# Kernel tuning notes

Measured on AMD Instinct MI355X. Metric: run time of the kernel, lower is better.

Reference implementation:

```python
import jax, jax.numpy as jnp
import numpy as np

N = 10000        # nodes
E = 160000       # edges (avg degree 16)
WIDTH = 32       # node hidden width
KER_W = 256      # kernel MLP hidden width
KER_IN = 6       # edge feature dim
DEPTH = 4        # message-passing iterations


def setup_inputs() -> dict:
    key = jax.random.key(0)
    ks = jax.random.split(key, 12)
    def w(k, shape, fan_in):
        return jax.random.normal(k, shape, jnp.float32) * (1.0 / np.sqrt(fan_in)).astype(np.float32)
    return {
        "x": jax.random.normal(ks[0], (N, 1), jnp.float32),
        "edge_index": jax.random.randint(ks[1], (2, E), 0, N),
        "edge_attr": jax.random.uniform(ks[2], (E, KER_IN), dtype=jnp.float32),
        # fc1: Linear(1, WIDTH)
        "fc1_w": w(ks[3], (1, WIDTH), 1), "fc1_b": jnp.zeros((WIDTH,), jnp.float32),
        # kernel DenseNet: KER_IN -> KER_W -> KER_W -> WIDTH^2 (ReLU between, none after last)
        "k1_w": w(ks[4], (KER_IN, KER_W), KER_IN), "k1_b": jnp.zeros((KER_W,), jnp.float32),
        "k2_w": w(ks[5], (KER_W, KER_W), KER_W), "k2_b": jnp.zeros((KER_W,), jnp.float32),
        "k3_w": w(ks[6], (KER_W, WIDTH * WIDTH), KER_W), "k3_b": jnp.zeros((WIDTH * WIDTH,), jnp.float32),
        # NNConv root weight + bias
        "root_w": w(ks[7], (WIDTH, WIDTH), WIDTH), "conv_b": jnp.zeros((WIDTH,), jnp.float32),
        # fc2: Linear(WIDTH, 1)
        "fc2_w": w(ks[8], (WIDTH, 1), WIDTH), "fc2_b": jnp.zeros((1,), jnp.float32),
    }


def reference(x, edge_index, edge_attr, fc1_w, fc1_b, k1_w, k1_b, k2_w, k2_b,
              k3_w, k3_b, root_w, conv_b, fc2_w, fc2_b):
    src, dst = edge_index[0], edge_index[1]  # messages flow src -> dst

    # Per-edge kernel weights (edge_attr is constant across depth -> compute once).
    h = jax.nn.relu(edge_attr @ k1_w + k1_b)
    h = jax.nn.relu(h @ k2_w + k2_b)
    W_e = (h @ k3_w + k3_b).reshape(E, WIDTH, WIDTH)  # [E, in, out]

    # Degree for scatter-mean (avoid div by zero).
    deg = jax.ops.segment_sum(jnp.ones((E,), jnp.float32), dst, num_segments=N)
    inv_deg = (1.0 / jnp.maximum(deg, 1.0))[:, None]

    h_node = x @ fc1_w + fc1_b  # [N, WIDTH]
    for _ in range(DEPTH):
        msg = jnp.einsum('ei,eio->eo', h_node[src], W_e)              # gather + per-edge GEMM
        agg = jax.ops.segment_sum(msg, dst, num_segments=N) * inv_deg  # scatter-mean
        h_node = jax.nn.relu(agg + h_node @ root_w + conv_b)
    return h_node @ fc2_w + fc2_b  # [N, 1]
```

## Files before the change

kernel.cpp:

```cpp
#include <hip/hip_runtime.h>
#include <hip/hip_fp16.h>

#define NNODE 10000
#define NEDGE 160000
#define W32 32
#define BSTR 40
#define PANEL_F16 10240
#define PANEL3_F16 5120
#define UB_TILES 20000
#define HB_STR 264
#define TB_STR 1036

typedef _Float16 f16;
typedef _Float16 f16x4 __attribute__((ext_vector_type(4)));
typedef _Float16 f16x8 __attribute__((ext_vector_type(8)));
typedef float f32x4 __attribute__((ext_vector_type(4)));

__device__ __forceinline__ void stage_panel(f16* lds, const f16* g, int w, int lane) {
    #pragma unroll
    for (int i = 0; i < 5; ++i) {
        int slot = w * 320 + i * 64 + lane;
        __builtin_amdgcn_global_load_lds(
            (const __attribute__((address_space(1))) unsigned int*)(g + (size_t)slot * 8),
            (__attribute__((address_space(3))) unsigned int*)(lds + (size_t)(w * 320 + i * 64) * 8),
            16, 0, 0);
    }
}

__device__ __forceinline__ void stage_panel10k(f16* lds, const f16* g, int w, int lane) {
    #pragma unroll
    for (int i = 0; i < 2; ++i) {
        int base = i * 256 + w * 64;
        __builtin_amdgcn_global_load_lds(
            (const __attribute__((address_space(1))) unsigned int*)(g + (size_t)(base + lane) * 8),
            (__attribute__((address_space(3))) unsigned int*)(lds + (size_t)base * 8),
            16, 0, 0);
    }
    if (w < 2) {
        int base = 512 + w * 64;
        __builtin_amdgcn_global_load_lds(
            (const __attribute__((address_space(1))) unsigned int*)(g + (size_t)(base + lane) * 8),
            (__attribute__((address_space(3))) unsigned int*)(lds + (size_t)base * 8),
            16, 0, 0);
    }
}

__global__ __launch_bounds__(256) void pack_k1(const float* __restrict__ k1w, f16* __restrict__ k1p) {
    int t = blockIdx.x * 256 + threadIdx.x;
    int j = t / BSTR, c = t % BSTR;
    k1p[t] = (c < 6) ? (f16)k1w[c * 256 + j] : (f16)0.f;
}
__global__ __launch_bounds__(256) void pack_k2(const float* __restrict__ k2w, f16* __restrict__ k2p) {
    int t = blockIdx.x * 256 + threadIdx.x;
    int kk = t / PANEL_F16, r = t % PANEL_F16;
    int j = r / BSTR, c = r % BSTR;
    k2p[t] = (c < 32) ? (f16)k2w[(size_t)(kk * 32 + c) * 256 + j] : (f16)0.f;
}
__global__ __launch_bounds__(256) void pack_k3(const float* __restrict__ k3w, f16* __restrict__ k3p) {
    int t = blockIdx.x * 256 + threadIdx.x;
    int p = t / PANEL3_F16, r = t % PANEL3_F16;
    int np = p >> 3, kk = p & 7;
    int j = r / BSTR, c = r % BSTR;
    k3p[t] = (c < 32) ? (f16)k3w[(size_t)(kk * 32 + c) * 1024 + np * 128 + j] : (f16)0.f;
}
__global__ __launch_bounds__(256) void pack_k3t(const float* __restrict__ k3w, f16* __restrict__ k3t) {
    int t = blockIdx.x * 256 + threadIdx.x;
    int q = t / BSTR, i = t % BSTR;
    int o = q >> 8, c = q & 255;
    k3t[t] = (i < 32) ? (f16)k3w[(size_t)c * 1024 + i * 32 + o] : (f16)0.f;
}

__global__ __launch_bounds__(256) void h2_kernel(
    const float* __restrict__ ea,
    const f16* __restrict__ k1p, const float* __restrict__ k1b,
    const f16* __restrict__ k2p, const float* __restrict__ k2b,
    f16* __restrict__ h2c, int e_start, const int* __restrict__ remap)
{
    __shared__ __align__(16) f16 bls[2][256 * BSTR];
    __shared__ __align__(16) f16 ea_s[64 * BSTR];
    __shared__ __align__(16) f16 hbuf[64 * HB_STR];

    const int t = threadIdx.x, w = t >> 6, lane = t & 63, quad = lane >> 4, l15 = lane & 15;
    const int el0 = blockIdx.x * 64;
    const int e0 = e_start + el0;

    stage_panel(bls[0], k1p, w, lane);
    for (int i = t; i < 64 * BSTR; i += 256) {
        int e = i / BSTR, c = i % BSTR;
        ea_s[i] = (f16)((c < 6) ? ea[(size_t)(e0 + e) * 6 + c] : 0.f);
    }
    __syncthreads();

    f16x8 a1 = *(const f16x8*)&ea_s[(w * 16 + l15) * BSTR + quad * 8];
    {
        f32x4 acc1[16];
        #pragma unroll
        for (int nt = 0; nt < 16; ++nt) { float b = k1b[nt * 16 + l15]; acc1[nt] = (f32x4){b, b, b, b}; }
        stage_panel(bls[1], k2p, w, lane);
        #pragma unroll
        for (int nt = 0; nt < 16; ++nt) {
            f16x8 bf = *(const f16x8*)&bls[0][(nt * 16 + l15) * BSTR + quad * 8];
            acc1[nt] = __builtin_amdgcn_mfma_f32_16x16x32_f16(a1, bf, acc1[nt], 0, 0, 0);
        }
        #pragma unroll
        for (int nt = 0; nt < 16; ++nt)
            #pragma unroll
            for (int r = 0; r < 4; ++r)
                hbuf[(w * 16 + quad * 4 + r) * HB_STR + nt * 16 + l15] = (f16)fmaxf(acc1[nt][r], 0.f);
    }
    __syncthreads();

    const int mh = w & 1, nh = w >> 1;
    f16x8 a2[2][8];
    #pragma unroll
    for (int m = 0; m < 2; ++m)
        #pragma unroll
        for (int kk = 0; kk < 8; ++kk)
            a2[m][kk] = *(const f16x8*)&hbuf[(mh * 32 + m * 16 + l15) * HB_STR + kk * 32 + quad * 8];
    f32x4 acc[2][8];
    #pragma unroll
    for (int nt = 0; nt < 8; ++nt) {
        float b = k2b[nh * 128 + nt * 16 + l15];
        acc[0][nt] = (f32x4){b, b, b, b};
        acc[1][nt] = (f32x4){b, b, b, b};
    }
    for (int kk = 0; kk < 8; ++kk) {
        if (kk < 7)
            stage_panel(bls[kk & 1], k2p + (size_t)(kk + 1) * PANEL_F16, w, lane);
        const f16* B = bls[(kk + 1) & 1];
        #pragma unroll
        for (int nt = 0; nt < 8; ++nt) {
            f16x8 bf = *(const f16x8*)&B[(nh * 128 + nt * 16 + l15) * BSTR + quad * 8];
            acc[0][nt] = __builtin_amdgcn_mfma_f32_16x16x32_f16(a2[0][kk], bf, acc[0][nt], 0, 0, 0);
            acc[1][nt] = __builtin_amdgcn_mfma_f32_16x16x32_f16(a2[1][kk], bf, acc[1][nt], 0, 0, 0);
        }
        __syncthreads();
    }
    size_t orow[2][4];
    #pragma unroll
    for (int m = 0; m < 2; ++m)
        #pragma unroll
        for (int r = 0; r < 4; ++r) {
            int row = mh * 32 + m * 16 + quad * 4 + r;
            orow[m][r] = remap ? (size_t)remap[e0 + row] : (size_t)(el0 + row);
        }
    #pragma unroll
    for (int m = 0; m < 2; ++m)
        #pragma unroll
        for (int nt = 0; nt < 8; ++nt)
            #pragma unroll
            for (int r = 0; r < 4; ++r)
                h2c[orow[m][r] * 256 + nh * 128 + nt * 16 + l15] = (f16)fmaxf(acc[m][nt][r], 0.f);
}

__global__ __launch_bounds__(256) void hist_kernel(const int* __restrict__ ei, int* __restrict__ cnt) {
    int e = blockIdx.x * 256 + threadIdx.x;
    if (e < NEDGE) atomicAdd(&cnt[ei[e]], 1);
}
__global__ __launch_bounds__(256) void scan_kernel(
    const int* __restrict__ cnt, int* __restrict__ edgeStart,
    int* __restrict__ tileStartN, int* __restrict__ cursor)
{
    __shared__ int pE[256], pT[256];
    const int t = threadIdx.x;
    int se = 0, st = 0;
    for (int k = 0; k < 40; ++k) {
        int n = t * 40 + k;
        if (n < NNODE) { int c = cnt[n]; se += c; st += (c + 15) >> 4; }
    }
    pE[t] = se; pT[t] = st;
    __syncthreads();
    if (t == 0) {
        int aE = 0, aT = 0;
        for (int i = 0; i < 256; ++i) { int tE = pE[i], tT = pT[i]; pE[i] = aE; pT[i] = aT; aE += tE; aT += tT; }
        tileStartN[NNODE] = aT;
    }
    __syncthreads();
    int oE = pE[t], oT = pT[t];
    for (int k = 0; k < 40; ++k) {
        int n = t * 40 + k;
        if (n < NNODE) {
            edgeStart[n] = oE; cursor[n] = oE; tileStartN[n] = oT;
            int c = cnt[n]; oE += c; oT += (c + 15) >> 4;
        }
    }
}
__global__ __launch_bounds__(256) void scatter_kernel(
    const int* __restrict__ ei, int* __restrict__ cursor,
    int* __restrict__ dstS, int* __restrict__ sortpos)
{
    int e = blockIdx.x * 256 + threadIdx.x;
    if (e < NEDGE) {
        int s = ei[e];
        int p = atomicAdd(&cursor[s], 1);
        dstS[p] = ei[NEDGE + e];
        sortpos[e] = p;
    }
}
__global__ __launch_bounds__(256) void tiles_kernel(
    const int* __restrict__ cnt, const int* __restrict__ edgeStart, const int* __restrict__ tileStartN,
    int* __restrict__ tileNode, int* __restrict__ tileE0, int* __restrict__ tileCnt)
{
    int n = blockIdx.x * 256 + threadIdx.x;
    if (n < NNODE) {
        int d = cnt[n], t0 = tileStartN[n], e0 = edgeStart[n];
        for (int k = 0; k * 16 < d; ++k) {
            int rem = d - k * 16;
            tileNode[t0 + k] = n;
            tileE0[t0 + k] = e0 + k * 16;
            tileCnt[t0 + k] = rem < 16 ? rem : 16;
        }
    }
}

__global__ __launch_bounds__(256) void h0_kernel(
    const float* __restrict__ x, const float* __restrict__ fc1w,
    const float* __restrict__ fc1b, float* __restrict__ h,
    const float* __restrict__ k3b, float* __restrict__ Bb)
{
    int idx = blockIdx.x * 256 + threadIdx.x;
    int n = idx >> 5, j = idx & 31;
    float hv = x[n] * fc1w[j] + fc1b[j];
    h[idx] = hv;
    float s = 0.f;
    #pragma unroll
    for (int i = 0; i < 32; ++i)
        s += __shfl(hv, i, 32) * k3b[i * 32 + j];
    Bb[idx] = s;
}

__global__ __launch_bounds__(256) void tgen_kernel(
    const float* __restrict__ h, const f16* __restrict__ k3t, f16* __restrict__ Tt,
    int n0, int n1)
{
    __shared__ __align__(16) f16 tbuf[16 * TB_STR];

    const int t = threadIdx.x, w = t >> 6, lane = t & 63, quad = lane >> 4, l15 = lane & 15;
    const int nBase = n0 + blockIdx.x * 16;
    const int colBase = blockIdx.y * 1024;

    f16x8 a;
    #pragma unroll
    for (int i = 0; i < 8; ++i) a[i] = (f16)0.f;
    int node = nBase + l15;
    if (node < n1) {
        const float4* hp = (const float4*)(h + (size_t)node * 32) + quad * 2;
        float4 v0 = hp[0], v1 = hp[1];
        a[0] = (f16)v0.x; a[1] = (f16)v0.y; a[2] = (f16)v0.z; a[3] = (f16)v0.w;
        a[4] = (f16)v1.x; a[5] = (f16)v1.y; a[6] = (f16)v1.z; a[7] = (f16)v1.w;
    }
    f32x4 acc[16];
    #pragma unroll
    for (int nt = 0; nt < 16; ++nt) {
        f16x8 bf = *(const f16x8*)&k3t[(size_t)(colBase + w * 256 + nt * 16 + l15) * BSTR + quad * 8];
        acc[nt] = __builtin_amdgcn_mfma_f32_16x16x32_f16(a, bf, (f32x4){0.f, 0.f, 0.f, 0.f}, 0, 0, 0);
    }
    #pragma unroll
    for (int nt = 0; nt < 16; ++nt)
        #pragma unroll
        for (int r = 0; r < 4; ++r)
            tbuf[(quad * 4 + r) * TB_STR + w * 256 + nt * 16 + l15] = (f16)acc[nt][r];
    __syncthreads();
    {
        const int row = t >> 4, u = t & 15;
        const int nd = nBase + row;
        if (nd < n1) {
            f16* gdst = Tt + (size_t)(nd - n0) * 8192 + colBase;
            const f16* lsrc = &tbuf[row * TB_STR];
            #pragma unroll
            for (int j = 0; j < 8; ++j) {
                int p = u + 16 * j;
                *(f16x8*)(gdst + p * 8) = *(const f16x8*)(lsrc + p * 8);
            }
        }
    }
}

__global__ __launch_bounds__(256) void msgT_kernel(
    const f16* __restrict__ h2s, const f16* __restrict__ Tt, const float* __restrict__ Bb,
    const int* __restrict__ tileNode, const int* __restrict__ tileE0, const int* __restrict__ tileCnt,
    const int* __restrict__ tileStartN, const int* __restrict__ dstS, float* __restrict__ agg,
    int n0, int n1)
{
    const int t = threadIdx.x, w = t >> 6, lane = t & 63, quad = lane >> 4, l15 = lane & 15;
    const int t0 = tileStartN[n0], t1 = tileStartN[n1];
    for (int tile = t0 + blockIdx.x * 4 + w; tile < t1; tile += gridDim.x * 4) {
        int n = tileNode[tile];
        int e0 = tileE0[tile], cnt = tileCnt[tile];
        const f16* Tn = Tt + (size_t)(n - n0) * 8192;
        f32x4 acc[2];
        #pragma unroll
        for (int nt = 0; nt < 2; ++nt) {
            float b = Bb[n * 32 + nt * 16 + l15];
            acc[nt] = (f32x4){b, b, b, b};
        }
        #pragma unroll
        for (int kk = 0; kk < 8; ++kk) {
            f16x8 a;
            #pragma unroll
            for (int i = 0; i < 8; ++i) a[i] = (f16)0.f;
            if (l15 < cnt)
                a = *(const f16x8*)&h2s[(size_t)(e0 + l15) * 256 + kk * 32 + quad * 8];
            #pragma unroll
            for (int nt = 0; nt < 2; ++nt) {
                f16x8 bf = *(const f16x8*)&Tn[(nt * 16 + l15) * 256 + kk * 32 + quad * 8];
                acc[nt] = __builtin_amdgcn_mfma_f32_16x16x32_f16(a, bf, acc[nt], 0, 0, 0);
            }
        }
        #pragma unroll
        for (int nt = 0; nt < 2; ++nt)
            #pragma unroll
            for (int r = 0; r < 4; ++r) {
                int er = quad * 4 + r;
                if (er < cnt)
                    atomicAdd(&agg[(size_t)dstS[e0 + er] * 32 + nt * 16 + l15], acc[nt][r]);
            }
    }
}

__global__ __launch_bounds__(256, 2) void msg_fused(
    const int* __restrict__ ei, const f16* __restrict__ h2c,
    const f16* __restrict__ k3p, const float* __restrict__ k3b,
    const float* __restrict__ h, float* __restrict__ agg, int e_start)
{
    __shared__ __align__(16) f16 bls[2][PANEL3_F16];
    __shared__ __align__(16) f16 h_s[256 * 36];
    __shared__ int dst_s[256];

    const int t = threadIdx.x, w = t >> 6, lane = t & 63, quad = lane >> 4, l15 = lane & 15;
    const int el0 = blockIdx.x * 256;
    const int e0 = e_start + el0;

    dst_s[t] = ei[NEDGE + e0 + t];
    {
        int srcn = ei[e0 + t];
        const float4* hr = (const float4*)(h + (size_t)srcn * 32);
        f16* dp = &h_s[t * 36];
        #pragma unroll
        for (int qq = 0; qq < 8; ++qq) {
            float4 v = hr[qq];
            dp[qq * 4 + 0] = (f16)v.x; dp[qq * 4 + 1] = (f16)v.y;
            dp[qq * 4 + 2] = (f16)v.z; dp[qq * 4 + 3] = (f16)v.w;
        }
    }
    stage_panel10k(bls[0], k3p, w, lane);

    float msg[4][4][2];
    #pragma unroll
    for (int m = 0; m < 4; ++m)
        #pragma unroll
        for (int r = 0; r < 4; ++r) { msg[m][r][0] = 0.f; msg[m][r][1] = 0.f; }

    f32x4 acc[4][8];
    __syncthreads();

    for (int it = 0; it < 64; ++it) {
        const int np = it >> 3, kk = it & 7;
        if (it) __syncthreads();
        if (it < 63) stage_panel10k(bls[(it + 1) & 1], k3p + (size_t)(it + 1) * PANEL3_F16, w, lane);

        f16x8 a[4];
        #pragma unroll
        for (int m = 0; m < 4; ++m)
            a[m] = *(const f16x8*)(h2c + (size_t)(el0 + w * 64 + m * 16 + l15) * 256 + kk * 32 + quad * 8);

        if (kk == 0) {
            #pragma unroll
            for (int nt = 0; nt < 8; ++nt) {
                float b = k3b[np * 128 + nt * 16 + l15];
                #pragma unroll
                for (int m = 0; m < 4; ++m) acc[m][nt] = (f32x4){b, b, b, b};
            }
        }
        const f16* B = bls[it & 1];
        #pragma unroll
        for (int nt = 0; nt < 8; ++nt) {
            f16x8 bf = *(const f16x8*)&B[(nt * 16 + l15) * BSTR + quad * 8];
            #pragma unroll
            for (int m = 0; m < 4; ++m)
                acc[m][nt] = __builtin_amdgcn_mfma_f32_16x16x32_f16(a[m], bf, acc[m][nt], 0, 0, 0);
        }
        if (kk == 7) {
            #pragma unroll
            for (int m = 0; m < 4; ++m)
                #pragma unroll
                for (int r = 0; r < 4; ++r) {
                    int row = w * 64 + m * 16 + quad * 4 + r;
                    f16x4 h4 = *(const f16x4*)&h_s[row * 36 + np * 4];
                    #pragma unroll
                    for (int nt = 0; nt < 8; ++nt)
                        msg[m][r][nt & 1] += (float)h4[nt >> 1] * acc[m][nt][r];
                }
        }
    }
    #pragma unroll
    for (int m = 0; m < 4; ++m)
        #pragma unroll
        for (int r = 0; r < 4; ++r) {
            int d = dst_s[w * 64 + m * 16 + quad * 4 + r];
            atomicAdd(&agg[d * W32 + l15],      msg[m][r][0]);
            atomicAdd(&agg[d * W32 + 16 + l15], msg[m][r][1]);
        }
}

__global__ __launch_bounds__(256) void deg_kernel(
    const int* __restrict__ ei, float* __restrict__ deg)
{
    int e = blockIdx.x * 256 + threadIdx.x;
    if (e < NEDGE) atomicAdd(&deg[ei[NEDGE + e]], 1.f);
}

__global__ __launch_bounds__(256) void update_kernel(
    const float* __restrict__ h_old, float* __restrict__ h_new,
    float* __restrict__ agg, const float* __restrict__ deg,
    const float* __restrict__ rootw, const float* __restrict__ convb,
    const float* __restrict__ k3b, float* __restrict__ Bb)
{
    __shared__ float rw[W32][W32 + 1];
    const int t = threadIdx.x;
    for (int q = t; q < W32 * W32; q += 256)
        rw[q >> 5][q & 31] = rootw[q];
    __syncthreads();
    const int nl = t >> 5, j = t & 31;
    const int n = blockIdx.x * 8 + nl;
    float hv = h_old[n * W32 + j];
    float acc = convb[j];
    #pragma unroll
    for (int k = 0; k < W32; ++k)
        acc += __shfl(hv, k, 32) * rw[k][j];
    float inv = 1.f / fmaxf(deg[n], 1.f);
    int idx = n * W32 + j;
    float a = agg[idx];
    agg[idx] = 0.f;
    float hn = fmaxf(a * inv + acc, 0.f);
    h_new[idx] = hn;
    float s = 0.f;
    #pragma unroll
    for (int i = 0; i < 32; ++i)
        s += __shfl(hn, i, 32) * k3b[i * 32 + j];
    Bb[idx] = s;
}

__global__ __launch_bounds__(256) void update_fb_kernel(
    const float* __restrict__ h_old, float* __restrict__ h_new,
    float* __restrict__ agg, const float* __restrict__ deg,
    const float* __restrict__ rootw, const float* __restrict__ convb)
{
    __shared__ float rw[W32][W32 + 1];
    const int t = threadIdx.x;
    for (int q = t; q < W32 * W32; q += 256)
        rw[q >> 5][q & 31] = rootw[q];
    __syncthreads();
    const int nl = t >> 5, j = t & 31;
    const int n = blockIdx.x * 8 + nl;
    float hv = h_old[n * W32 + j];
    float acc = convb[j];
    #pragma unroll
    for (int k = 0; k < W32; ++k)
        acc += __shfl(hv, k, 32) * rw[k][j];
    float inv = 1.f / fmaxf(deg[n], 1.f);
    int idx = n * W32 + j;
    float a = agg[idx];
    agg[idx] = 0.f;
    h_new[idx] = fmaxf(a * inv + acc, 0.f);
}

__global__ __launch_bounds__(256) void out_kernel(
    const float* __restrict__ h, const float* __restrict__ fc2w,
    const float* __restrict__ fc2b, float* __restrict__ out)
{
    int n = blockIdx.x * 256 + threadIdx.x;
    if (n < NNODE) {
        float a = fc2b[0];
        #pragma unroll
        for (int j = 0; j < W32; ++j)
            a += h[n * W32 + j] * fc2w[j];
        out[n] = a;
    }
}

static inline size_t pad256(size_t x) { return (x + 255) & ~(size_t)255; }

extern "C" void kernel_launch(void* const* d_in, const int* in_sizes, int n_in,
                              void* d_out, int out_size, void* d_ws, size_t ws_size,
                              hipStream_t stream) {
    const float* x    = (const float*)d_in[0];
    const int*   ei   = (const int*)  d_in[1];
    const float* ea   = (const float*)d_in[2];
    const float* fc1w = (const float*)d_in[3];
    const float* fc1b = (const float*)d_in[4];
    const float* k1w  = (const float*)d_in[5];
    const float* k1b  = (const float*)d_in[6];
    const float* k2w  = (const float*)d_in[7];
    const float* k2b  = (const float*)d_in[8];
    const float* k3w  = (const float*)d_in[9];
    const float* k3b  = (const float*)d_in[10];
    const float* rootw= (const float*)d_in[11];
    const float* convb= (const float*)d_in[12];
    const float* fc2w = (const float*)d_in[13];
    const float* fc2b = (const float*)d_in[14];
    float* out = (float*)d_out;

    const size_t hbytes = (size_t)NNODE * W32 * 4;
    char* ws = (char*)d_ws;
    size_t off = 0;
    float* hA  = (float*)(ws + off); off += hbytes;
    float* hB  = (float*)(ws + off); off += hbytes;
    float* agg = (float*)(ws + off); off += hbytes;
    float* deg = (float*)(ws + off); off += 40960;
    f16*  k1p  = (f16*)(ws + off);   off += 20480;
    f16*  k2p  = (f16*)(ws + off);   off += 163840;
    f16*  k3p  = (f16*)(ws + off);   off += 655360;
    const size_t fixed = off;

    size_t toff = fixed;
    f16*  k3t      = (f16*)(ws + toff);  toff += pad256(8192 * BSTR * 2);
    int*  dstS     = (int*)(ws + toff);  toff += pad256((size_t)NEDGE * 4);
    int*  sortpos  = (int*)(ws + toff);  toff += pad256((size_t)NEDGE * 4);
    int*  cnt      = (int*)(ws + toff);  toff += pad256((size_t)NNODE * 4);
    int*  edgeStart= (int*)(ws + toff);  toff += pad256((size_t)NNODE * 4);
    int*  tileStartN=(int*)(ws + toff);  toff += pad256((size_t)(NNODE + 1) * 4);
    int*  cursor   = (int*)(ws + toff);  toff += pad256((size_t)NNODE * 4);
    int*  tileNode = (int*)(ws + toff);  toff += pad256((size_t)UB_TILES * 4);
    int*  tileE0   = (int*)(ws + toff);  toff += pad256((size_t)UB_TILES * 4);
    int*  tileCnt  = (int*)(ws + toff);  toff += pad256((size_t)UB_TILES * 4);
    float* Bb      = (float*)(ws + toff); toff += pad256((size_t)NNODE * 32 * 4);
    f16*  h2s      = (f16*)(ws + toff);  toff += pad256((size_t)NEDGE * 256 * 2);
    f16*  Tt       = (f16*)(ws + toff);

    int nc = 0, CS = 0;
    {
        const int cands[4] = {1, 2, 4, 8};
        for (int ci = 0; ci < 4; ++ci) {
            int c = cands[ci];
            int cs = ((NNODE + c - 1) / c + 15) & ~15;
            size_t tb = (size_t)cs * 8192 * 2;
            if (ws_size >= toff + tb) { nc = c; CS = cs; break; }
        }
    }

    hipMemsetAsync(deg, 0, (size_t)NNODE * 4, stream);
    hipMemsetAsync(agg, 0, (size_t)NNODE * W32 * 4, stream);

    pack_k1<<<40, 256, 0, stream>>>(k1w, k1p);
    pack_k2<<<320, 256, 0, stream>>>(k2w, k2p);

    h0_kernel<<<NNODE * W32 / 256, 256, 0, stream>>>(x, fc1w, fc1b, hA, k3b, Bb);
    deg_kernel<<<(NEDGE + 255) / 256, 256, 0, stream>>>(ei, deg);

    float* hcur = hA; float* hnext = hB;

    if (nc) {
        pack_k3t<<<1280, 256, 0, stream>>>(k3w, k3t);
        hipMemsetAsync(cnt, 0, (size_t)NNODE * 4, stream);
        hist_kernel<<<(NEDGE + 255) / 256, 256, 0, stream>>>(ei, cnt);
        scan_kernel<<<1, 256, 0, stream>>>(cnt, edgeStart, tileStartN, cursor);
        scatter_kernel<<<(NEDGE + 255) / 256, 256, 0, stream>>>(ei, cursor, dstS, sortpos);
        tiles_kernel<<<(NNODE + 255) / 256, 256, 0, stream>>>(cnt, edgeStart, tileStartN,
                                                              tileNode, tileE0, tileCnt);
        h2_kernel<<<NEDGE / 64, 256, 0, stream>>>(ea, k1p, k1b, k2p, k2b, h2s, 0, sortpos);

        for (int d = 0; d < 4; ++d) {
            for (int ct = 0; ct < nc; ++ct) {
                int n0 = ct * CS;
                if (n0 >= NNODE) break;
                int n1 = n0 + CS; if (n1 > NNODE) n1 = NNODE;
                dim3 tg((n1 - n0 + 15) / 16, 8);
                tgen_kernel<<<tg, 256, 0, stream>>>(hcur, k3t, Tt, n0, n1);
                msgT_kernel<<<1280, 256, 0, stream>>>(h2s, Tt, Bb, tileNode, tileE0, tileCnt,
                                                      tileStartN, dstS, agg, n0, n1);
            }
            update_kernel<<<NNODE / 8, 256, 0, stream>>>(hcur, hnext, agg, deg, rootw, convb,
                                                         k3b, Bb);
            float* tmp = hcur; hcur = hnext; hnext = tmp;
        }
    } else {
        f16* h2b = (f16*)(ws + fixed);
        pack_k3<<<1280, 256, 0, stream>>>(k3w, k3p);

        long long availC = 0;
        if (ws_size > fixed) availC = (long long)((ws_size - fixed) / 512);
        int C = (availC > NEDGE) ? NEDGE : (int)availC;
        C &= ~255;
        if (C < 256) return;

        const bool full = (C == NEDGE);
        if (full)
            h2_kernel<<<NEDGE / 64, 256, 0, stream>>>(ea, k1p, k1b, k2p, k2b, h2b, 0, nullptr);

        for (int d = 0; d < 4; ++d) {
            for (int es = 0; es < NEDGE; es += C) {
                int ce = (NEDGE - es < C) ? (NEDGE - es) : C;
                if (!full)
                    h2_kernel<<<ce / 64, 256, 0, stream>>>(ea, k1p, k1b, k2p, k2b, h2b, es, nullptr);
                msg_fused<<<ce / 256, 256, 0, stream>>>(ei, h2b, k3p, k3b, hcur, agg, es);
            }
            update_fb_kernel<<<NNODE / 8, 256, 0, stream>>>(hcur, hnext, agg, deg, rootw, convb);
            float* tmp = hcur; hcur = hnext; hnext = tmp;
        }
    }
    out_kernel<<<(NNODE + 255) / 256, 256, 0, stream>>>(hcur, fc2w, fc2b, out);
}
```

Before: 611.1 us.

## Assign one wave per source node and keep its T panel in registers

The tile-list indirection (tiles_kernel, tileStartN and the tile arrays) is removed. msgT now iterates per source node with a wave-strided loop. Each wave loads the node's 32x256 T panel into registers once and reuses it across all 16-edge chunks of that node, rather than reloading it for every tile. This cuts redundant T loads and a setup kernel. The cost is more registers for the held fragments and coarser load balance, since high-degree nodes now fall to a single wave.

```diff
diff --git a/kernel.cpp b/kernel.cpp
--- a/kernel.cpp
+++ b/kernel.cpp
@@ -7,7 +7,6 @@
 #define BSTR 40
 #define PANEL_F16 10240
 #define PANEL3_F16 5120
-#define UB_TILES 20000
 #define HB_STR 264
 #define TB_STR 1036
 
@@ -158,30 +157,28 @@
     if (e < NEDGE) atomicAdd(&cnt[ei[e]], 1);
 }
 __global__ __launch_bounds__(256) void scan_kernel(
-    const int* __restrict__ cnt, int* __restrict__ edgeStart,
-    int* __restrict__ tileStartN, int* __restrict__ cursor)
-{
-    __shared__ int pE[256], pT[256];
+    const int* __restrict__ cnt, int* __restrict__ edgeStart, int* __restrict__ cursor)
+{
+    __shared__ int pE[256];
     const int t = threadIdx.x;
-    int se = 0, st = 0;
+    int se = 0;
     for (int k = 0; k < 40; ++k) {
         int n = t * 40 + k;
-        if (n < NNODE) { int c = cnt[n]; se += c; st += (c + 15) >> 4; }
-    }
-    pE[t] = se; pT[t] = st;
+        if (n < NNODE) se += cnt[n];
+    }
+    pE[t] = se;
     __syncthreads();
     if (t == 0) {
-        int aE = 0, aT = 0;
-        for (int i = 0; i < 256; ++i) { int tE = pE[i], tT = pT[i]; pE[i] = aE; pT[i] = aT; aE += tE; aT += tT; }
-        tileStartN[NNODE] = aT;
-    }
-    __syncthreads();
-    int oE = pE[t], oT = pT[t];
+        int aE = 0;
+        for (int i = 0; i < 256; ++i) { int tE = pE[i]; pE[i] = aE; aE += tE; }
+    }
+    __syncthreads();
+    int oE = pE[t];
     for (int k = 0; k < 40; ++k) {
         int n = t * 40 + k;
         if (n < NNODE) {
-            edgeStart[n] = oE; cursor[n] = oE; tileStartN[n] = oT;
-            int c = cnt[n]; oE += c; oT += (c + 15) >> 4;
+            edgeStart[n] = oE; cursor[n] = oE;
+            oE += cnt[n];
         }
     }
 }
@@ -195,21 +192,6 @@
         int p = atomicAdd(&cursor[s], 1);
         dstS[p] = ei[NEDGE + e];
         sortpos[e] = p;
-    }
-}
-__global__ __launch_bounds__(256) void tiles_kernel(
-    const int* __restrict__ cnt, const int* __restrict__ edgeStart, const int* __restrict__ tileStartN,
-    int* __restrict__ tileNode, int* __restrict__ tileE0, int* __restrict__ tileCnt)
-{
-    int n = blockIdx.x * 256 + threadIdx.x;
-    if (n < NNODE) {
-        int d = cnt[n], t0 = tileStartN[n], e0 = edgeStart[n];
-        for (int k = 0; k * 16 < d; ++k) {
-            int rem = d - k * 16;
-            tileNode[t0 + k] = n;
-            tileE0[t0 + k] = e0 + k * 16;
-            tileCnt[t0 + k] = rem < 16 ? rem : 16;
-        }
     }
 }
 
@@ -278,43 +260,48 @@
 
 __global__ __launch_bounds__(256) void msgT_kernel(
     const f16* __restrict__ h2s, const f16* __restrict__ Tt, const float* __restrict__ Bb,
-    const int* __restrict__ tileNode, const int* __restrict__ tileE0, const int* __restrict__ tileCnt,
-    const int* __restrict__ tileStartN, const int* __restrict__ dstS, float* __restrict__ agg,
+    const int* __restrict__ cnt, const int* __restrict__ edgeStart,
+    const int* __restrict__ dstS, float* __restrict__ agg,
     int n0, int n1)
 {
     const int t = threadIdx.x, w = t >> 6, lane = t & 63, quad = lane >> 4, l15 = lane & 15;
-    const int t0 = tileStartN[n0], t1 = tileStartN[n1];
-    for (int tile = t0 + blockIdx.x * 4 + w; tile < t1; tile += gridDim.x * 4) {
-        int n = tileNode[tile];
-        int e0 = tileE0[tile], cnt = tileCnt[tile];
+    const int gw = blockIdx.x * 4 + w, nw = gridDim.x * 4;
+    for (int n = n0 + gw; n < n1; n += nw) {
+        const int deg = cnt[n];
+        if (deg == 0) continue;
+        const int e0 = edgeStart[n];
         const f16* Tn = Tt + (size_t)(n - n0) * 8192;
-        f32x4 acc[2];
-        #pragma unroll
-        for (int nt = 0; nt < 2; ++nt) {
-            float b = Bb[n * 32 + nt * 16 + l15];
-            acc[nt] = (f32x4){b, b, b, b};
-        }
-        #pragma unroll
-        for (int kk = 0; kk < 8; ++kk) {
-            f16x8 a;
-            #pragma unroll
-            for (int i = 0; i < 8; ++i) a[i] = (f16)0.f;
-            if (l15 < cnt)
-                a = *(const f16x8*)&h2s[(size_t)(e0 + l15) * 256 + kk * 32 + quad * 8];
-            #pragma unroll
-            for (int nt = 0; nt < 2; ++nt) {
-                f16x8 bf = *(const f16x8*)&Tn[(nt * 16 + l15) * 256 + kk * 32 + quad * 8];
-                acc[nt] = __builtin_amdgcn_mfma_f32_16x16x32_f16(a, bf, acc[nt], 0, 0, 0);
+        f16x8 bf[2][8];
+        #pragma unroll
+        for (int nt = 0; nt < 2; ++nt)
+            #pragma unroll
+            for (int kk = 0; kk < 8; ++kk)
+                bf[nt][kk] = *(const f16x8*)&Tn[(nt * 16 + l15) * 256 + kk * 32 + quad * 8];
+        const float b0 = Bb[n * 32 + l15], b1 = Bb[n * 32 + 16 + l15];
+        for (int eb = 0; eb < deg; eb += 16) {
+            const int c = (deg - eb < 16) ? (deg - eb) : 16;
+            f32x4 acc0 = (f32x4){b0, b0, b0, b0};
+            f32x4 acc1 = (f32x4){b1, b1, b1, b1};
+            #pragma unroll
+            for (int kk = 0; kk < 8; ++kk) {
+                f16x8 a;
+                #pragma unroll
+                for (int i = 0; i < 8; ++i) a[i] = (f16)0.f;
+                if (l15 < c)
+                    a = *(const f16x8*)&h2s[(size_t)(e0 + eb + l15) * 256 + kk * 32 + quad * 8];
+                acc0 = __builtin_amdgcn_mfma_f32_16x16x32_f16(a, bf[0][kk], acc0, 0, 0, 0);
+                acc1 = __builtin_amdgcn_mfma_f32_16x16x32_f16(a, bf[1][kk], acc1, 0, 0, 0);
             }
-        }
-        #pragma unroll
-        for (int nt = 0; nt < 2; ++nt)
             #pragma unroll
             for (int r = 0; r < 4; ++r) {
                 int er = quad * 4 + r;
-                if (er < cnt)
-                    atomicAdd(&agg[(size_t)dstS[e0 + er] * 32 + nt * 16 + l15], acc[nt][r]);
+                if (er < c) {
+                    int d = dstS[e0 + eb + er];
+                    atomicAdd(&agg[(size_t)d * 32 + l15],      acc0[r]);
+                    atomicAdd(&agg[(size_t)d * 32 + 16 + l15], acc1[r]);
+                }
             }
+        }
     }
 }
 
@@ -519,11 +506,7 @@
     int*  sortpos  = (int*)(ws + toff);  toff += pad256((size_t)NEDGE * 4);
     int*  cnt      = (int*)(ws + toff);  toff += pad256((size_t)NNODE * 4);
     int*  edgeStart= (int*)(ws + toff);  toff += pad256((size_t)NNODE * 4);
-    int*  tileStartN=(int*)(ws + toff);  toff += pad256((size_t)(NNODE + 1) * 4);
     int*  cursor   = (int*)(ws + toff);  toff += pad256((size_t)NNODE * 4);
-    int*  tileNode = (int*)(ws + toff);  toff += pad256((size_t)UB_TILES * 4);
-    int*  tileE0   = (int*)(ws + toff);  toff += pad256((size_t)UB_TILES * 4);
-    int*  tileCnt  = (int*)(ws + toff);  toff += pad256((size_t)UB_TILES * 4);
     float* Bb      = (float*)(ws + toff); toff += pad256((size_t)NNODE * 32 * 4);
     f16*  h2s      = (f16*)(ws + toff);  toff += pad256((size_t)NEDGE * 256 * 2);
     f16*  Tt       = (f16*)(ws + toff);
@@ -554,10 +537,8 @@
         pack_k3t<<<1280, 256, 0, stream>>>(k3w, k3t);
         hipMemsetAsync(cnt, 0, (size_t)NNODE * 4, stream);
         hist_kernel<<<(NEDGE + 255) / 256, 256, 0, stream>>>(ei, cnt);
-        scan_kernel<<<1, 256, 0, stream>>>(cnt, edgeStart, tileStartN, cursor);
+        scan_kernel<<<1, 256, 0, stream>>>(cnt, edgeStart, cursor);
         scatter_kernel<<<(NEDGE + 255) / 256, 256, 0, stream>>>(ei, cursor, dstS, sortpos);
-        tiles_kernel<<<(NNODE + 255) / 256, 256, 0, stream>>>(cnt, edgeStart, tileStartN,
-                                                              tileNode, tileE0, tileCnt);
         h2_kernel<<<NEDGE / 64, 256, 0, stream>>>(ea, k1p, k1b, k2p, k2b, h2s, 0, sortpos);
 
         for (int d = 0; d < 4; ++d) {
@@ -567,8 +548,8 @@
                 int n1 = n0 + CS; if (n1 > NNODE) n1 = NNODE;
                 dim3 tg((n1 - n0 + 15) / 16, 8);
                 tgen_kernel<<<tg, 256, 0, stream>>>(hcur, k3t, Tt, n0, n1);
-                msgT_kernel<<<1280, 256, 0, stream>>>(h2s, Tt, Bb, tileNode, tileE0, tileCnt,
-                                                      tileStartN, dstS, agg, n0, n1);
+                msgT_kernel<<<1280, 256, 0, stream>>>(h2s, Tt, Bb, cnt, edgeStart,
+                                                      dstS, agg, n0, n1);
             }
             update_kernel<<<NNODE / 8, 256, 0, stream>>>(hcur, hnext, agg, deg, rootw, convb,
                                                          k3b, Bb);
```

New measurement: 622.3 us. Within noise of the previous version (+1.8%).
